# Kernel optimization log

Hardware: AMD Instinct MI355X
Metric: run time of the kernel (lower is better)

The kernel has to match this reference:

```python
import jax, jax.numpy as jnp
import numpy as np

N_HEAD = 16
N_KV_HEADS = 4
HEAD_SIZE = 128  # n_embd // n_head = 2048 // 16


def setup_inputs() -> dict:
    key = jax.random.key(0)
    k0, k1, k2 = jax.random.split(key, 3)
    B, T, C = 4, 2048, 2048
    kv_dim = N_KV_HEADS * HEAD_SIZE  # 512
    x = jax.random.normal(k0, (B, T, C), dtype=jnp.float32)
    W_attn = jax.random.normal(k1, (C, C + 2 * kv_dim), dtype=jnp.float32) * 0.02
    b_attn = jnp.zeros((C + 2 * kv_dim,), dtype=jnp.float32)
    W_proj = jax.random.normal(k2, (C, C), dtype=jnp.float32) * 0.02
    b_proj = jnp.zeros((C,), dtype=jnp.float32)
    return {"x": x, "W_attn": W_attn, "b_attn": b_attn, "W_proj": W_proj, "b_proj": b_proj}


def reference(x, W_attn, b_attn, W_proj, b_proj):
    B, T, C = x.shape
    hs = HEAD_SIZE
    kv_dim = N_KV_HEADS * hs
    qkv = x @ W_attn + b_attn                      # [B,T,C+2*kv_dim]
    q, k, v = jnp.split(qkv, [C, C + kv_dim], axis=2)
    q = q.reshape(B, T, N_HEAD, hs).transpose(0, 2, 1, 3)       # [B,H,T,hs]
    k = k.reshape(B, T, N_KV_HEADS, hs).transpose(0, 2, 1, 3)   # [B,Hkv,T,hs]
    v = v.reshape(B, T, N_KV_HEADS, hs).transpose(0, 2, 1, 3)
    # GQA: repeat_interleave kv heads to match query heads
    rep = N_HEAD // N_KV_HEADS
    k_r = jnp.repeat(k, rep, axis=1)               # [B,H,T,hs]
    v_r = jnp.repeat(v, rep, axis=1)
    scale = 1.0 / jnp.sqrt(jnp.float32(hs))
    scores = jnp.einsum('bhqd,bhkd->bhqk', q, k_r) * scale      # [B,H,T,T]
    causal = jnp.tril(jnp.ones((T, T), dtype=bool))
    scores = jnp.where(causal, scores, jnp.finfo(scores.dtype).min)
    attn = jax.nn.softmax(scores, axis=-1)
    y = jnp.einsum('bhqk,bhkd->bhqd', attn, v_r)   # [B,H,T,hs]
    y = y.transpose(0, 2, 1, 3).reshape(B, T, C)
    y = y @ W_proj + b_proj
    return y
```

## Files before the change

kernel.cpp:

```cpp
#include <hip/hip_runtime.h>
#include <stdint.h>

#define DEVI __device__ __forceinline__

typedef __attribute__((ext_vector_type(8))) uint16_t u16x8;
typedef __attribute__((ext_vector_type(4))) uint16_t u16x4v;
typedef __attribute__((ext_vector_type(4))) uint32_t u32x4;
typedef __attribute__((ext_vector_type(8))) __bf16 bf16x8;
typedef __attribute__((ext_vector_type(4))) float f32x4;
typedef __attribute__((ext_vector_type(16))) float f32x16;

DEVI uint16_t f2bf(float x) {
  union { float f; uint32_t u; } v; v.f = x;
  return (uint16_t)((v.u + 0x7fffu + ((v.u >> 16) & 1u)) >> 16);
}

DEVI uint16_t f2bfn(float f) {
  __bf16 h = (__bf16)f;
  return __builtin_bit_cast(uint16_t, h);
}

DEVI f32x4 mfma16(u16x8 a, u16x8 b, f32x4 c) {
  return __builtin_amdgcn_mfma_f32_16x16x32_bf16(
      __builtin_bit_cast(bf16x8, a), __builtin_bit_cast(bf16x8, b), c, 0, 0, 0);
}

DEVI f32x16 mfma32(u16x8 a, u16x8 b, f32x16 c) {
  return __builtin_amdgcn_mfma_f32_32x32x16_bf16(
      __builtin_bit_cast(bf16x8, a), __builtin_bit_cast(bf16x8, b), c, 0, 0, 0);
}

DEVI void async16(void* lds, const void* g) {
  __builtin_amdgcn_global_load_lds(
      (const __attribute__((address_space(1))) uint32_t*)g,
      (__attribute__((address_space(3))) uint32_t*)lds, 16, 0, 0);
}

#define QSC 0.12751742925f

__global__ void cvt_f32_bf16(const float* __restrict__ in, uint16_t* __restrict__ out, int n4) {
  int i = blockIdx.x * blockDim.x + threadIdx.x;
  const int st = gridDim.x * blockDim.x;
  for (; i < n4; i += st) {
    float4 v = ((const float4*)in)[i];
    u16x4v o;
    o[0] = f2bf(v.x); o[1] = f2bf(v.y); o[2] = f2bf(v.z); o[3] = f2bf(v.w);
    ((u16x4v*)out)[i] = o;
  }
}

__global__ void transp_cvt(const float* __restrict__ in, uint16_t* __restrict__ out,
                           int K, int N) {
  __shared__ float Ws[64][65];
  const int n0 = blockIdx.x * 64, k0 = blockIdx.y * 64;
  const int t = threadIdx.x;
  const int r = t >> 4, c = (t & 15) << 2;
#pragma unroll
  for (int it = 0; it < 4; ++it) {
    float4 v = *(const float4*)&in[(size_t)(k0 + it * 16 + r) * N + n0 + c];
    Ws[it * 16 + r][c] = v.x; Ws[it * 16 + r][c + 1] = v.y;
    Ws[it * 16 + r][c + 2] = v.z; Ws[it * 16 + r][c + 3] = v.w;
  }
  __syncthreads();
#pragma unroll
  for (int it = 0; it < 4; ++it) {
    const int rr = it * 16 + r;
    const int cc = c;
    ushort4 o;
    o.x = f2bf(Ws[cc][rr]);     o.y = f2bf(Ws[cc + 1][rr]);
    o.z = f2bf(Ws[cc + 2][rr]); o.w = f2bf(Ws[cc + 3][rr]);
    *(ushort4*)&out[(size_t)(n0 + rr) * K + k0 + cc] = o;
  }
}

__global__ __launch_bounds__(512, 1)
void gemm_qkv(const uint16_t* __restrict__ A, const uint16_t* __restrict__ Bt,
              const float* __restrict__ bias,
              uint16_t* __restrict__ q, uint16_t* __restrict__ kk, uint16_t* __restrict__ vt,
              int M, int N, int K) {
  constexpr int BK = 64;
  __shared__ uint16_t As[2][256 * BK];
  __shared__ uint16_t Bs[2][128 * BK];
  int bid = (int)blockIdx.x;
  const int q8 = (int)gridDim.x >> 3;
  bid = (bid & 7) * q8 + (bid >> 3);
  const int nbn = N >> 7;
  const int brow = (bid / nbn) << 8;
  const int bcol = (bid % nbn) << 7;
  const int t = threadIdx.x;
  const int wid = t >> 6, lane = t & 63;
  const int wm = wid >> 1, wn = wid & 1;
  const int lr = lane & 15, g = lane >> 4, l7 = lr & 7;

  const int logch = (((t & 7) ^ ((t >> 3) & 7)) << 3);
  const uint16_t* Asrc = A + (size_t)(brow + (t >> 3)) * K + logch;
  const uint16_t* Bsrc = Bt + (size_t)(bcol + (t >> 3)) * K + logch;
  const size_t skip64 = (size_t)64 * K;
  const int dt = t * 8;

  auto stageA = [&](int buf, int k0) {
#pragma unroll
    for (int l = 0; l < 4; ++l)
      async16(&As[buf][l * 4096 + dt], Asrc + (size_t)l * skip64 + k0);
  };
  auto stageB = [&](int buf, int k0) {
#pragma unroll
    for (int l = 0; l < 2; ++l)
      async16(&Bs[buf][l * 4096 + dt], Bsrc + (size_t)l * skip64 + k0);
  };

  f32x4 acc[4][4];
#pragma unroll
  for (int i = 0; i < 4; ++i)
#pragma unroll
    for (int j = 0; j < 4; ++j) acc[i][j] = f32x4{0.f, 0.f, 0.f, 0.f};

  const int nt = K / BK;
  stageA(0, 0); stageB(0, 0);
  if (nt > 1) stageB(1, BK);
  asm volatile("s_waitcnt vmcnt(0)" ::: "memory");
  __builtin_amdgcn_s_barrier();

  for (int tt = 0; tt < nt; ++tt) {
    const int buf = tt & 1;
    u16x8 bfr[4][2];
#pragma unroll
    for (int p = 0; p < 2; ++p) {
      if (p == 0) {
#pragma unroll
        for (int j = 0; j < 4; ++j) {
          const int brw = wn * 64 + j * 16 + lr;
#pragma unroll
          for (int s = 0; s < 2; ++s)
            bfr[j][s] = *(const u16x8*)&Bs[buf][brw * 64 + ((((s << 2) + g) ^ l7) << 3)];
        }
      }
      u16x8 af[2][2];
#pragma unroll
      for (int ii = 0; ii < 2; ++ii) {
        const int arow = wm * 64 + (p * 2 + ii) * 16 + lr;
#pragma unroll
        for (int s = 0; s < 2; ++s)
          af[ii][s] = *(const u16x8*)&As[buf][arow * 64 + ((((s << 2) + g) ^ l7) << 3)];
      }
      if (p == 0) {
        if (tt + 1 < nt) stageA(buf ^ 1, (tt + 1) * BK);
      } else {
        if (tt + 2 < nt) {
          stageB(buf, (tt + 2) * BK);
          asm volatile("s_waitcnt vmcnt(2)" ::: "memory");
        } else {
          asm volatile("s_waitcnt vmcnt(0)" ::: "memory");
        }
      }
      __builtin_amdgcn_s_barrier();
      __builtin_amdgcn_s_setprio(1);
#pragma unroll
      for (int ii = 0; ii < 2; ++ii)
#pragma unroll
        for (int j = 0; j < 4; ++j)
#pragma unroll
          for (int s = 0; s < 2; ++s)
            acc[p * 2 + ii][j] = mfma16(af[ii][s], bfr[j][s], acc[p * 2 + ii][j]);
      __builtin_amdgcn_s_setprio(0);
      __builtin_amdgcn_s_barrier();
    }
  }

#pragma unroll
  for (int i = 0; i < 4; ++i) {
#pragma unroll
    for (int j = 0; j < 4; ++j) {
      const int col = bcol + wn * 64 + j * 16 + lr;
      const float bb = bias[col];
      const int rowb = brow + wm * 64 + i * 16 + (g << 2);
      const int b_ = rowb >> 11, ttb = rowb & 2047;
      const int d = col & 127;
      float vals[4];
#pragma unroll
      for (int r = 0; r < 4; ++r) vals[r] = acc[i][j][r] + bb;
      if (col < 2048) {
        const int hh = col >> 7;
#pragma unroll
        for (int r = 0; r < 4; ++r)
          q[((size_t)((b_ * 16 + hh) * 2048 + ttb + r) << 7) + d] = f2bf(vals[r] * QSC);
      } else if (col < 2560) {
        const int hh = (col - 2048) >> 7;
#pragma unroll
        for (int r = 0; r < 4; ++r)
          kk[((size_t)((b_ * 4 + hh) * 2048 + ttb + r) << 7) + d] = f2bf(vals[r]);
      } else {
        const int hh = (col - 2560) >> 7;
        u16x4v pk;
#pragma unroll
        for (int r = 0; r < 4; ++r) pk[r] = f2bf(vals[r]);
        *(u16x4v*)&vt[(((size_t)((b_ * 4 + hh) * 128 + d)) << 11) + ttb] = pk;
      }
    }
  }
}

__global__ __launch_bounds__(512, 1)
void gemm_proj(const uint16_t* __restrict__ A, const uint16_t* __restrict__ Bt,
               const float* __restrict__ bias, float* __restrict__ outF,
               int M, int N, int K) {
  constexpr int BK = 64;
  __shared__ uint16_t As[2][256 * BK];
  __shared__ uint16_t Bs[2][256 * BK];
  int bid = (int)blockIdx.x;
  const int q8 = (int)gridDim.x >> 3;
  bid = (bid & 7) * q8 + (bid >> 3);
  const int nbn = N >> 8;
  const int brow = (bid / nbn) << 8;
  const int bcol = (bid % nbn) << 8;
  const int t = threadIdx.x;
  const int wid = t >> 6, lane = t & 63;
  const int wm = wid >> 2, wn = wid & 3;
  const int lr = lane & 15, g = lane >> 4;
  const int l7 = lr & 7;

  const int sr0 = t >> 3;
  const int logch = (((t & 7) ^ ((t >> 3) & 7)) << 3);
  const uint16_t* Asrc0 = A + (size_t)(brow + sr0) * K + logch;
  const uint16_t* Asrc1 = A + (size_t)(brow + 64 + sr0) * K + logch;
  const uint16_t* Bsrc0 = Bt + (size_t)(bcol + sr0) * K + logch;
  const uint16_t* Bsrc1 = Bt + (size_t)(bcol + 64 + sr0) * K + logch;
  const size_t hskip = (size_t)128 * K;
  const int d0 = t * 8, d1 = 4096 + t * 8;

  auto stageA = [&](int buf, int h, int k0) {
    async16(&As[buf][h * 8192 + d0], Asrc0 + (size_t)h * hskip + k0);
    async16(&As[buf][h * 8192 + d1], Asrc1 + (size_t)h * hskip + k0);
  };
  auto stageB = [&](int buf, int h, int k0) {
    async16(&Bs[buf][h * 8192 + d0], Bsrc0 + (size_t)h * hskip + k0);
    async16(&Bs[buf][h * 8192 + d1], Bsrc1 + (size_t)h * hskip + k0);
  };

  f32x4 acc[8][4];
#pragma unroll
  for (int i = 0; i < 8; ++i)
#pragma unroll
    for (int j = 0; j < 4; ++j) acc[i][j] = f32x4{0.f, 0.f, 0.f, 0.f};

  const int nt = K / BK;
  stageA(0, 0, 0); stageA(0, 1, 0);
  stageB(0, 0, 0); stageB(0, 1, 0);
  if (nt > 1) { stageB(1, 0, BK); stageB(1, 1, BK); }
  asm volatile("s_waitcnt vmcnt(0)" ::: "memory");
  __builtin_amdgcn_s_barrier();

  for (int tt = 0; tt < nt; ++tt) {
    const int buf = tt & 1;
    u16x8 bfr[4][2];
#pragma unroll
    for (int p = 0; p < 4; ++p) {
      if (p == 0) {
#pragma unroll
        for (int j = 0; j < 4; ++j) {
          const int brw = wn * 64 + j * 16 + lr;
#pragma unroll
          for (int s = 0; s < 2; ++s)
            bfr[j][s] = *(const u16x8*)&Bs[buf][brw * 64 + ((((s << 2) + g) ^ l7) << 3)];
        }
      }
      u16x8 af[2][2];
#pragma unroll
      for (int ii = 0; ii < 2; ++ii) {
        const int arow = wm * 128 + (p * 2 + ii) * 16 + lr;
#pragma unroll
        for (int s = 0; s < 2; ++s)
          af[ii][s] = *(const u16x8*)&As[buf][arow * 64 + ((((s << 2) + g) ^ l7) << 3)];
      }
      if (p == 0) { if (tt + 1 < nt) stageA(buf ^ 1, 0, (tt + 1) * BK); }
      if (p == 1) { if (tt + 1 < nt) stageA(buf ^ 1, 1, (tt + 1) * BK); }
      if (p == 2) { if (tt + 2 < nt) stageB(buf, 0, (tt + 2) * BK); }
      if (p == 3) {
        if (tt + 2 < nt) {
          stageB(buf, 1, (tt + 2) * BK);
          asm volatile("s_waitcnt vmcnt(4)" ::: "memory");
        } else {
          asm volatile("s_waitcnt vmcnt(0)" ::: "memory");
        }
      }
      __builtin_amdgcn_s_barrier();
      __builtin_amdgcn_s_setprio(1);
#pragma unroll
      for (int ii = 0; ii < 2; ++ii)
#pragma unroll
        for (int j = 0; j < 4; ++j)
#pragma unroll
          for (int s = 0; s < 2; ++s)
            acc[p * 2 + ii][j] = mfma16(af[ii][s], bfr[j][s], acc[p * 2 + ii][j]);
      __builtin_amdgcn_s_setprio(0);
      __builtin_amdgcn_s_barrier();
    }
  }

#pragma unroll
  for (int i = 0; i < 8; ++i) {
#pragma unroll
    for (int j = 0; j < 4; ++j) {
      const int col = bcol + wn * 64 + j * 16 + lr;
      const float bb = bias[col];
#pragma unroll
      for (int r = 0; r < 4; ++r) {
        const int row = brow + wm * 128 + i * 16 + (g << 2) + r;
        outF[(size_t)row * N + col] = acc[i][j][r] + bb;
      }
    }
  }
}

__global__ __launch_bounds__(512, 1)
void attn_fwd(const uint16_t* __restrict__ Q,
              const uint16_t* __restrict__ Kg,
              const uint16_t* __restrict__ Vt,
              uint16_t* __restrict__ Y,
              int T) {
  __shared__ __align__(16) uint16_t Ks[2][64 * 128];
  __shared__ __align__(16) uint16_t Vs[128 * 64];
  const int id = (int)blockIdx.x;
  const int x = id & 7;
  const int h = (id >> 3) & 15, b = (id >> 7) & 3;
  const int qb = (id & 256) ? 7 - x : x;
  const int hkv = h >> 2;

  const int t = threadIdx.x, w = t >> 6, lane = t & 63;
  const int ql = lane & 31, b5 = lane >> 5;
  const int swzK = (ql & 15) << 3;
  const int swzV = (ql & 7) << 3;

  const uint16_t* Qp = Q + ((size_t)(b * 16 + h) * T + qb * 256) * 128;
  const uint16_t* Kp = Kg + (size_t)(b * 4 + hkv) * T * 128;
  const uint16_t* Vp = Vt + (size_t)(b * 4 + hkv) * 128 * T;

  auto stageK = [&](int buf, int kv0) {
#pragma unroll
    for (int l = 0; l < 2; ++l) {
      const int s = l * 512 + t;
      const int row = s >> 4;
      const int cl = (s & 15) ^ (row & 15);
      async16(&Ks[buf][s * 8], &Kp[(size_t)(kv0 + row) * 128 + cl * 8]);
    }
  };
  auto stageV = [&](int kv0) {
#pragma unroll
    for (int l = 0; l < 2; ++l) {
      const int s = l * 512 + t;
      const int row = s >> 3;
      const int cl = (s & 7) ^ (row & 7);
      async16(&Vs[s * 8], &Vp[(size_t)row * T + kv0 + cl * 8]);
    }
  };

  const int row0 = qb * 256 + w * 32;
  const int qrow = row0 + ql;

  u16x8 qf[8];
#pragma unroll
  for (int kc = 0; kc < 8; ++kc)
    qf[kc] = *(const u16x8*)&Qp[(size_t)(w * 32 + ql) * 128 + kc * 16 + b5 * 8];

  f32x16 o[4];
#pragma unroll
  for (int db = 0; db < 4; ++db)
#pragma unroll
    for (int r = 0; r < 16; ++r) o[db][r] = 0.f;
  float mrow = -3e38f, lrow = 0.f;

  const int ntiles = 4 * qb + 4;
  const int myn = 4 * qb + (w >> 1) + 1;

  stageK(0, 0);
  __syncthreads();

  int cur = 0;
  for (int tile = 0; tile < ntiles; ++tile) {
    const int kv0 = tile << 6;
    stageV(kv0);
    if (tile + 1 < ntiles) stageK(cur ^ 1, (tile + 1) << 6);

    const bool run = tile < myn;
    f32x16 s[2];
    u16x8 pa[4];
    if (run) {
#pragma unroll
      for (int m = 0; m < 2; ++m)
#pragma unroll
        for (int r = 0; r < 16; ++r) s[m][r] = 0.f;
      __builtin_amdgcn_s_setprio(1);
#pragma unroll
      for (int kc = 0; kc < 8; ++kc) {
        const int cc = (kc * 16 + b5 * 8) ^ swzK;
        u16x8 k0f = *(const u16x8*)&Ks[cur][ql * 128 + cc];
        u16x8 k1f = *(const u16x8*)&Ks[cur][(32 + ql) * 128 + cc];
        s[0] = mfma32(k0f, qf[kc], s[0]);
        s[1] = mfma32(k1f, qf[kc], s[1]);
      }
      __builtin_amdgcn_s_setprio(0);

      if (kv0 + 63 > row0) {
#pragma unroll
        for (int m = 0; m < 2; ++m)
#pragma unroll
          for (int r = 0; r < 16; ++r) {
            const int kg = kv0 + 32 * m + (r & 3) + 8 * (r >> 2) + 4 * b5;
            if (kg > qrow) s[m][r] = -3e38f;
          }
      }
      float mt[16];
#pragma unroll
      for (int r = 0; r < 16; ++r) mt[r] = fmaxf(s[0][r], s[1][r]);
#pragma unroll
      for (int st = 8; st >= 1; st >>= 1)
#pragma unroll
        for (int r = 0; r < st; ++r) mt[r] = fmaxf(mt[r], mt[r + st]);
      float mx = fmaxf(mt[0], __shfl_xor(mt[0], 32));
      const bool defer = __all(mx <= mrow + 8.f);
      const float mnew = defer ? mrow : fmaxf(mrow, mx);
      const float sc = defer ? 1.f : exp2f(mrow - mnew);
#pragma unroll
      for (int m = 0; m < 2; ++m)
#pragma unroll
        for (int r = 0; r < 16; ++r) s[m][r] = exp2f(s[m][r] - mnew);
      float pt[16];
#pragma unroll
      for (int r = 0; r < 16; ++r) pt[r] = s[0][r] + s[1][r];
#pragma unroll
      for (int st = 8; st >= 1; st >>= 1)
#pragma unroll
        for (int r = 0; r < st; ++r) pt[r] += pt[r + st];
      float ps = pt[0] + __shfl_xor(pt[0], 32);
      mrow = mnew;
      lrow = lrow * sc + ps;
      if (!defer) {
#pragma unroll
        for (int db = 0; db < 4; ++db)
#pragma unroll
          for (int r = 0; r < 16; ++r) o[db][r] *= sc;
      }

#pragma unroll
      for (int m = 0; m < 2; ++m) {
        uint32_t pw[4][2];
#pragma unroll
        for (int a = 0; a < 4; ++a)
#pragma unroll
          for (int hh = 0; hh < 2; ++hh)
            pw[a][hh] = (uint32_t)f2bfn(s[m][4 * a + 2 * hh]) |
                        ((uint32_t)f2bfn(s[m][4 * a + 2 * hh + 1]) << 16);
#pragma unroll
        for (int c = 0; c < 2; ++c) {
          uint32_t wd[4];
#pragma unroll
          for (int hh = 0; hh < 2; ++hh) {
            const uint32_t mine  = b5 ? pw[2 * c + 1][hh] : pw[2 * c][hh];
            const uint32_t yours = b5 ? pw[2 * c][hh] : pw[2 * c + 1][hh];
            const uint32_t xw = (uint32_t)__shfl_xor((int)yours, 32);
            wd[hh] = b5 ? xw : mine;
            wd[2 + hh] = b5 ? mine : xw;
          }
          u32x4 tmp = {wd[0], wd[1], wd[2], wd[3]};
          pa[2 * m + c] = __builtin_bit_cast(u16x8, tmp);
        }
      }
    }
    __syncthreads();

    if (run) {
      __builtin_amdgcn_s_setprio(1);
#pragma unroll
      for (int db = 0; db < 4; ++db) {
#pragma unroll
        for (int kf = 0; kf < 4; ++kf) {
          u16x8 vf = *(const u16x8*)&Vs[(32 * db + ql) * 64 +
                                        ((kf * 16 + b5 * 8) ^ swzV)];
          o[db] = mfma32(vf, pa[kf], o[db]);
        }
      }
      __builtin_amdgcn_s_setprio(0);
    }
    __syncthreads();
    cur ^= 1;
  }

  uint16_t* Yp = Y + ((size_t)(b * T + row0 + ql)) * 2048 + h * 128 + b5 * 4;
  const float inv = 1.f / lrow;
#pragma unroll
  for (int db = 0; db < 4; ++db)
#pragma unroll
    for (int a = 0; a < 4; ++a) {
      u16x4v pk;
#pragma unroll
      for (int r = 0; r < 4; ++r) pk[r] = f2bfn(o[db][4 * a + r] * inv);
      *(u16x4v*)&Yp[db * 32 + a * 8] = pk;
    }
}

extern "C" void kernel_launch(void* const* d_in, const int* in_sizes, int n_in,
                              void* d_out, int out_size, void* d_ws, size_t ws_size,
                              hipStream_t stream) {
  const float* x      = (const float*)d_in[0];
  const float* W_attn = (const float*)d_in[1];
  const float* b_attn = (const float*)d_in[2];
  const float* W_proj = (const float*)d_in[3];
  const float* b_proj = (const float*)d_in[4];
  float* out = (float*)d_out;

  const int B = 4, T = 2048, C = 2048, H = 16, HKV = 4, HS = 128;
  const int M = B * T;
  const int Nqkv = C + 2 * HKV * HS;

  uint8_t* ws = (uint8_t*)d_ws;
  size_t off = 0;
  auto alloc = [&](size_t bytes) {
    void* p = ws + off;
    off += (bytes + 255) & ~(size_t)255;
    return p;
  };
  uint16_t* xb  = (uint16_t*)alloc((size_t)M * C * 2);
  uint16_t* WaT = (uint16_t*)alloc((size_t)Nqkv * C * 2);
  uint16_t* WpT = (uint16_t*)alloc((size_t)C * C * 2);
  uint16_t* qb  = (uint16_t*)alloc((size_t)B * H * T * HS * 2);
  uint16_t* kb  = (uint16_t*)alloc((size_t)B * HKV * T * HS * 2);
  uint16_t* vtb = (uint16_t*)alloc((size_t)B * HKV * HS * T * 2);
  uint16_t* yb  = xb;

  cvt_f32_bf16<<<2048, 256, 0, stream>>>(x, xb, M * C / 4);
  transp_cvt<<<dim3(Nqkv / 64, C / 64), 256, 0, stream>>>(W_attn, WaT, C, Nqkv);
  transp_cvt<<<dim3(C / 64, C / 64), 256, 0, stream>>>(W_proj, WpT, C, C);
  gemm_qkv<<<dim3((M / 256) * (Nqkv / 128)), 512, 0, stream>>>(
      xb, WaT, b_attn, qb, kb, vtb, M, Nqkv, C);
  attn_fwd<<<dim3(512), 512, 0, stream>>>(qb, kb, vtb, yb, T);
  gemm_proj<<<dim3((M / 256) * (C / 256)), 512, 0, stream>>>(
      yb, WpT, b_proj, out, M, C, C);
}
```

Baseline: 334.2 us.

## Triple-buffer A tiles in QKV GEMM with two-tile-ahead prefetch

The QKV projection GEMM moves from double-buffering A in LDS to a three-slot ring. Both A and B for tile tt+2 are now issued together in the second half of each K iteration, and the wait only covers the loads for tile tt+1. The goal is to give global loads of A more time in flight and hide their latency behind the MFMA work. The cost is more LDS for the extra A slot, plus ring-index bookkeeping and six outstanding async loads per thread.

```diff
diff --git a/kernel.cpp b/kernel.cpp
--- a/kernel.cpp
+++ b/kernel.cpp
@@ -79,7 +79,7 @@
               uint16_t* __restrict__ q, uint16_t* __restrict__ kk, uint16_t* __restrict__ vt,
               int M, int N, int K) {
   constexpr int BK = 64;
-  __shared__ uint16_t As[2][256 * BK];
+  __shared__ uint16_t As[3][256 * BK];
   __shared__ uint16_t Bs[2][128 * BK];
   int bid = (int)blockIdx.x;
   const int q8 = (int)gridDim.x >> 3;
@@ -117,54 +117,67 @@
 
   const int nt = K / BK;
   stageA(0, 0); stageB(0, 0);
-  if (nt > 1) stageB(1, BK);
+  if (nt > 1) { stageA(1, BK); stageB(1, BK); }
   asm volatile("s_waitcnt vmcnt(0)" ::: "memory");
   __builtin_amdgcn_s_barrier();
 
+  int cA = 0;
   for (int tt = 0; tt < nt; ++tt) {
-    const int buf = tt & 1;
+    const int bbuf = tt & 1;
     u16x8 bfr[4][2];
 #pragma unroll
-    for (int p = 0; p < 2; ++p) {
-      if (p == 0) {
-#pragma unroll
-        for (int j = 0; j < 4; ++j) {
-          const int brw = wn * 64 + j * 16 + lr;
-#pragma unroll
-          for (int s = 0; s < 2; ++s)
-            bfr[j][s] = *(const u16x8*)&Bs[buf][brw * 64 + ((((s << 2) + g) ^ l7) << 3)];
-        }
-      }
-      u16x8 af[2][2];
-#pragma unroll
-      for (int ii = 0; ii < 2; ++ii) {
-        const int arow = wm * 64 + (p * 2 + ii) * 16 + lr;
+    for (int j = 0; j < 4; ++j) {
+      const int brw = wn * 64 + j * 16 + lr;
+#pragma unroll
+      for (int s = 0; s < 2; ++s)
+        bfr[j][s] = *(const u16x8*)&Bs[bbuf][brw * 64 + ((((s << 2) + g) ^ l7) << 3)];
+    }
+    u16x8 af[2][2];
+#pragma unroll
+    for (int ii = 0; ii < 2; ++ii) {
+      const int arow = wm * 64 + ii * 16 + lr;
+#pragma unroll
+      for (int s = 0; s < 2; ++s)
+        af[ii][s] = *(const u16x8*)&As[cA][arow * 64 + ((((s << 2) + g) ^ l7) << 3)];
+    }
+    __builtin_amdgcn_s_barrier();
+    __builtin_amdgcn_s_setprio(1);
+#pragma unroll
+    for (int ii = 0; ii < 2; ++ii)
+#pragma unroll
+      for (int j = 0; j < 4; ++j)
 #pragma unroll
         for (int s = 0; s < 2; ++s)
-          af[ii][s] = *(const u16x8*)&As[buf][arow * 64 + ((((s << 2) + g) ^ l7) << 3)];
-      }
-      if (p == 0) {
-        if (tt + 1 < nt) stageA(buf ^ 1, (tt + 1) * BK);
-      } else {
-        if (tt + 2 < nt) {
-          stageB(buf, (tt + 2) * BK);
-          asm volatile("s_waitcnt vmcnt(2)" ::: "memory");
-        } else {
-          asm volatile("s_waitcnt vmcnt(0)" ::: "memory");
-        }
-      }
-      __builtin_amdgcn_s_barrier();
-      __builtin_amdgcn_s_setprio(1);
-#pragma unroll
-      for (int ii = 0; ii < 2; ++ii)
-#pragma unroll
-        for (int j = 0; j < 4; ++j)
-#pragma unroll
-          for (int s = 0; s < 2; ++s)
-            acc[p * 2 + ii][j] = mfma16(af[ii][s], bfr[j][s], acc[p * 2 + ii][j]);
-      __builtin_amdgcn_s_setprio(0);
-      __builtin_amdgcn_s_barrier();
-    }
+          acc[ii][j] = mfma16(af[ii][s], bfr[j][s], acc[ii][j]);
+    __builtin_amdgcn_s_setprio(0);
+    __builtin_amdgcn_s_barrier();
+#pragma unroll
+    for (int ii = 0; ii < 2; ++ii) {
+      const int arow = wm * 64 + (2 + ii) * 16 + lr;
+#pragma unroll
+      for (int s = 0; s < 2; ++s)
+        af[ii][s] = *(const u16x8*)&As[cA][arow * 64 + ((((s << 2) + g) ^ l7) << 3)];
+    }
+    if (tt + 2 < nt) {
+      int cA2 = cA + 2; if (cA2 >= 3) cA2 -= 3;
+      stageA(cA2, (tt + 2) * BK);
+      stageB(bbuf, (tt + 2) * BK);
+      asm volatile("s_waitcnt vmcnt(6)" ::: "memory");
+    } else {
+      asm volatile("s_waitcnt vmcnt(0)" ::: "memory");
+    }
+    __builtin_amdgcn_s_barrier();
+    __builtin_amdgcn_s_setprio(1);
+#pragma unroll
+    for (int ii = 0; ii < 2; ++ii)
+#pragma unroll
+      for (int j = 0; j < 4; ++j)
+#pragma unroll
+        for (int s = 0; s < 2; ++s)
+          acc[2 + ii][j] = mfma16(af[ii][s], bfr[j][s], acc[2 + ii][j]);
+    __builtin_amdgcn_s_setprio(0);
+    __builtin_amdgcn_s_barrier();
+    cA = (cA + 1 == 3) ? 0 : cA + 1;
   }
 
 #pragma unroll
```

Measured after the change: 339.7 us. Within noise of the previous version (+1.6%).
